# Kernel optimization log

Measured on AMD Instinct MI355X. Metric: run time of the kernel, lower is better.

The kernel has to match this reference:

```python
import jax, jax.numpy as jnp
import numpy as np

N = 10000      # nodes
E = 100000     # edges
C = 32         # in_channels == hidden_channels == out_channels
ED = 4         # edge_dim
G = 64         # number of graphs in the batch
EPS = 1e-5     # BatchNorm eps


def setup_inputs() -> dict:
    key = jax.random.key(0)
    ks = jax.random.split(key, 20)
    rn = lambda k, shape, s=0.05: jax.random.normal(k, shape, dtype=jnp.float32) * s
    return {
        "x": jax.random.normal(ks[0], (N, C), dtype=jnp.float32),
        "edge_attr": jax.random.normal(ks[1], (E, ED), dtype=jnp.float32),
        # edge MLP 1: ED -> C -> C*C ; NNConv1 root/bias
        "e1_w1": rn(ks[2], (ED, C)), "e1_b1": jnp.zeros((C,), jnp.float32),
        "e1_w2": rn(ks[3], (C, C * C)), "e1_b2": jnp.zeros((C * C,), jnp.float32),
        "root1": rn(ks[4], (C, C)), "bias1": jnp.zeros((C,), jnp.float32),
        # edge MLP 2: ED -> C -> C*C ; NNConv2 root/bias
        "e2_w1": rn(ks[5], (ED, C)), "e2_b1": jnp.zeros((C,), jnp.float32),
        "e2_w2": rn(ks[6], (C, C * C)), "e2_b2": jnp.zeros((C * C,), jnp.float32),
        "root2": rn(ks[7], (C, C)), "bias2": jnp.zeros((C,), jnp.float32),
        # BatchNorm (eval mode: running stats)
        "bn1_g": jnp.ones((C,), jnp.float32), "bn1_b": jnp.zeros((C,), jnp.float32),
        "bn1_m": rn(ks[8], (C,), 0.1), "bn1_v": 1.0 + 0.1 * jax.random.uniform(ks[9], (C,), dtype=jnp.float32),
        "bn2_g": jnp.ones((C,), jnp.float32), "bn2_b": jnp.zeros((C,), jnp.float32),
        "bn2_m": rn(ks[10], (C,), 0.1), "bn2_v": 1.0 + 0.1 * jax.random.uniform(ks[11], (C,), dtype=jnp.float32),
        # readout: C -> C//2 -> 1
        "r1_w": rn(ks[12], (C, C // 2)), "r1_b": jnp.zeros((C // 2,), jnp.float32),
        "r2_w": rn(ks[13], (C // 2, 1)), "r2_b": jnp.zeros((1,), jnp.float32),
        "edge_index": jax.random.randint(ks[14], (2, E), 0, N),
        "batch": jnp.sort(jax.random.randint(ks[15], (N,), 0, G)),
    }


def _nnconv(x, edge_index, edge_attr, w1, b1, w2, b2, root, bias):
    # edge MLP -> per-edge weight matrix [E, C, C]
    h = jax.nn.relu(edge_attr @ w1 + b1)
    W = (h @ w2 + b2).reshape(E, C, C)
    src, dst = edge_index[0], edge_index[1]
    # gather source features, per-edge matmul, scatter-mean to target nodes
    msg = jnp.einsum('ei,eio->eo', x[src], W)                      # [E, C]
    agg = jax.ops.segment_sum(msg, dst, num_segments=N)            # [N, C]
    cnt = jax.ops.segment_sum(jnp.ones((E,), x.dtype), dst, num_segments=N)
    agg = agg / jnp.maximum(cnt, 1.0)[:, None]
    return agg + x @ root + bias


def _bn(x, g, b, m, v):
    return (x - m) * jax.lax.rsqrt(v + EPS) * g + b


def reference(x, edge_attr,
              e1_w1, e1_b1, e1_w2, e1_b2, root1, bias1,
              e2_w1, e2_b1, e2_w2, e2_b2, root2, bias2,
              bn1_g, bn1_b, bn1_m, bn1_v,
              bn2_g, bn2_b, bn2_m, bn2_v,
              r1_w, r1_b, r2_w, r2_b,
              edge_index, batch):
    h = jax.nn.relu(_bn(_nnconv(x, edge_index, edge_attr, e1_w1, e1_b1, e1_w2, e1_b2, root1, bias1),
                        bn1_g, bn1_b, bn1_m, bn1_v))
    h = jax.nn.relu(_bn(_nnconv(h, edge_index, edge_attr, e2_w1, e2_b1, e2_w2, e2_b2, root2, bias2),
                        bn2_g, bn2_b, bn2_m, bn2_v))
    # global mean pool over graphs
    psum = jax.ops.segment_sum(h, batch, num_segments=G)           # [G, C]
    pcnt = jax.ops.segment_sum(jnp.ones((N,), h.dtype), batch, num_segments=G)
    pooled = psum / jnp.maximum(pcnt, 1.0)[:, None]
    # readout MLP (dropout is identity in eval)
    return jax.nn.relu(pooled @ r1_w + r1_b) @ r2_w + r2_b          # [G, 1]
```

## Files before the change

### kernel.cpp

```cpp
#include <hip/hip_runtime.h>

#define NN 10000
#define EE 100000
#define CC 32
#define GG 64
#define EPSV 1e-5f
#define NB 8
#define SLOTS 1056
#define HST 32
#define PST 36
#define PNODE (32*PST)
#define EBLK (EE/8)
#define HBLK ((EE+255)/256)
#define WBLK 160

__global__ __launch_bounds__(256) void k_pre(const int* __restrict__ ei,
        int* __restrict__ cnt, int* __restrict__ deg,
        const float* __restrict__ w2a, const float* __restrict__ b2a,
        const float* __restrict__ w2b, const float* __restrict__ b2b,
        float* __restrict__ w2r1, float* __restrict__ w2r2) {
    int blk = blockIdx.x;
    int t = threadIdx.x;
    if (blk < HBLK) {
        int e = blk * 256 + t;
        if (e < EE) {
            atomicAdd(&cnt[ei[EE + e]], 1);
            atomicAdd(&deg[ei[e]], 1);
        }
    } else {
        int b2i = blk - HBLK;
        int s = (b2i % 5) * 256 + t;
        int i = b2i / 5;
        if (s < SLOTS) {
            float va = (s < 1024) ? w2a[(s >> 5) * 1024 + i * 32 + (s & 31)]
                                  : b2a[i * 32 + (s - 1024)];
            float vb = (s < 1024) ? w2b[(s >> 5) * 1024 + i * 32 + (s & 31)]
                                  : b2b[i * 32 + (s - 1024)];
            w2r1[i * SLOTS + s] = va;
            w2r2[i * SLOTS + s] = vb;
        }
    }
}

__global__ __launch_bounds__(1024) void k_scan(const int* __restrict__ deg,
                                               int* __restrict__ rowptr,
                                               int* __restrict__ cursor) {
    __shared__ int buf[1024];
    int t = threadIdx.x;
    int v[10]; int s = 0;
    int base = t * 10;
    #pragma unroll
    for (int k = 0; k < 10; k++) {
        int idx = base + k;
        v[k] = (idx < NN) ? deg[idx] : 0;
        s += v[k];
    }
    buf[t] = s;
    for (int off = 1; off < 1024; off <<= 1) {
        __syncthreads();
        int val = buf[t] + ((t >= off) ? buf[t - off] : 0);
        __syncthreads();
        buf[t] = val;
    }
    __syncthreads();
    int carry = (t > 0) ? buf[t - 1] : 0;
    #pragma unroll
    for (int k = 0; k < 10; k++) {
        int idx = base + k;
        if (idx < NN) { rowptr[idx] = carry; cursor[idx] = carry; }
        carry += v[k];
    }
    if (t == 1023) rowptr[NN] = buf[1023];
}

__global__ void k_scatter(const int* __restrict__ ei,
                          int* __restrict__ cursor, int* __restrict__ csr_eid,
                          int2* __restrict__ meta) {
    int e = blockIdx.x * blockDim.x + threadIdx.x;
    if (e >= EE) return;
    int s = ei[e];
    int d = ei[EE + e];
    int pos = atomicAdd(&cursor[s], 1);
    csr_eid[pos] = e;
    meta[pos] = make_int2(s, d);
}

__global__ __launch_bounds__(256) void k_h(const float* __restrict__ edge_attr,
        const float* __restrict__ w1a, const float* __restrict__ b1a,
        const float* __restrict__ w1b, const float* __restrict__ b1b,
        const int* __restrict__ csr_eid,
        float* __restrict__ hbuf1, float* __restrict__ hbuf2) {
    int t = threadIdx.x;
    int pos = blockIdx.x * 8 + (t >> 5);
    int o = t & 31;
    int e = csr_eid[pos];
    float4 a = *(const float4*)&edge_attr[(size_t)e * 4];
    float ha = fmaxf(a.x * w1a[o] + a.y * w1a[32 + o] + a.z * w1a[64 + o] + a.w * w1a[96 + o] + b1a[o], 0.f);
    float hb = fmaxf(a.x * w1b[o] + a.y * w1b[32 + o] + a.z * w1b[64 + o] + a.w * w1b[96 + o] + b1b[o], 0.f);
    hbuf1[(size_t)pos * HST + o] = ha;
    hbuf2[(size_t)pos * HST + o] = hb;
}

__global__ __launch_bounds__(256, 3) void k_fused3(const float* __restrict__ x,
        const float* __restrict__ hbuf,
        const float* __restrict__ w2r,
        const int2* __restrict__ meta, const int* __restrict__ rowptr,
        float* __restrict__ agg) {
    __shared__ float xs[NB][32];
    __shared__ float P2[NB * PNODE];
    int t = threadIdx.x;
    int o = t & 31;
    int cb = 4 * (t >> 5);
    int n0 = blockIdx.x * NB;

    xs[t >> 5][t & 31] = x[n0 * 32 + t];
    __syncthreads();

    {
        float acc[4][NB];
        #pragma unroll
        for (int k = 0; k < 4; k++)
            #pragma unroll
            for (int n = 0; n < NB; n++) acc[k][n] = 0.f;
        #pragma unroll
        for (int j = 0; j < 8; j++) {
            float wk[4][4];
            #pragma unroll
            for (int r = 0; r < 4; r++)
                #pragma unroll
                for (int k = 0; k < 4; k++)
                    wk[r][k] = w2r[(4 * j + r) * SLOTS + (cb + k) * 32 + o];
            #pragma unroll
            for (int n = 0; n < NB; n++) {
                float4 xq = *(const float4*)&xs[n][4 * j];
                #pragma unroll
                for (int k = 0; k < 4; k++)
                    acc[k][n] += xq.x * wk[0][k] + xq.y * wk[1][k]
                               + xq.z * wk[2][k] + xq.w * wk[3][k];
            }
        }
        #pragma unroll
        for (int n = 0; n < NB; n++) {
            float4 st = make_float4(acc[0][n], acc[1][n], acc[2][n], acc[3][n]);
            *(float4*)&P2[n * PNODE + o * PST + cb] = st;
        }
    }
    if (t < 32) {
        float wb[32];
        #pragma unroll
        for (int i = 0; i < 32; i++) wb[i] = w2r[i * SLOTS + 1024 + t];
        #pragma unroll
        for (int n = 0; n < NB; n++) {
            float b = 0.f;
            #pragma unroll
            for (int j = 0; j < 8; j++) {
                float4 xq = *(const float4*)&xs[n][4 * j];
                b += xq.x * wb[4 * j] + xq.y * wb[4 * j + 1]
                   + xq.z * wb[4 * j + 2] + xq.w * wb[4 * j + 3];
            }
            *(float4*)&P2[n * PNODE + t * PST + 32] = make_float4(b, 0.f, 0.f, 0.f);
        }
    }
    __syncthreads();

    int ebase = rowptr[n0];
    int eend  = rowptr[n0 + NB];
    int grp = t >> 5;
    int pos = ebase + grp;
    int src_c = 0, dst_c = 0;
    float4 hq[8];
    if (pos < eend) {
        int2 sd = meta[pos];
        src_c = sd.x; dst_c = sd.y;
        const float* hb = &hbuf[(size_t)pos * HST];
        #pragma unroll
        for (int b = 0; b < 8; b++) hq[b] = *(const float4*)&hb[4 * b];
    }
    while (pos < eend) {
        int pos_n = pos + 8;
        int src_n = 0, dst_n = 0;
        float4 hq_n[8];
        if (pos_n < eend) {
            int2 sd = meta[pos_n];
            src_n = sd.x; dst_n = sd.y;
            const float* hbn = &hbuf[(size_t)pos_n * HST];
            #pragma unroll
            for (int b = 0; b < 8; b++) hq_n[b] = *(const float4*)&hbn[4 * b];
        }
        const float* Pn = &P2[(src_c - n0) * PNODE + o * PST];
        float msg = Pn[32];
        #pragma unroll
        for (int b = 0; b < 8; b++) {
            float4 pq = *(const float4*)&Pn[4 * b];
            msg += hq[b].x * pq.x + hq[b].y * pq.y
                 + hq[b].z * pq.z + hq[b].w * pq.w;
        }
        atomicAdd(&agg[(size_t)dst_c * 32 + o], msg);
        pos = pos_n; src_c = src_n; dst_c = dst_n;
        #pragma unroll
        for (int b = 0; b < 8; b++) hq[b] = hq_n[b];
    }
}

__global__ __launch_bounds__(256) void k_combine(const float* __restrict__ x_in,
        float* __restrict__ agg, const int* __restrict__ cnt,
        const float* __restrict__ root, const float* __restrict__ bias,
        const float* __restrict__ bng, const float* __restrict__ bnb,
        const float* __restrict__ bnm, const float* __restrict__ bnv,
        float* __restrict__ x_out, float* __restrict__ psum,
        const int* __restrict__ batch) {
    __shared__ float xs[8][32];
    __shared__ float vals[8][32];
    __shared__ int gb[8];
    int t = threadIdx.x;
    int n0 = blockIdx.x * 8;
    xs[t >> 5][t & 31] = x_in[n0 * 32 + t];
    __syncthreads();
    int k = t >> 5, o = t & 31, n = n0 + k;
    float r = bias[o];
    #pragma unroll
    for (int i = 0; i < 32; i++) r += xs[k][i] * root[i * 32 + o];
    float a = agg[(size_t)n * 32 + o] / fmaxf((float)cnt[n], 1.f);
    float val = a + r;
    val = (val - bnm[o]) * rsqrtf(bnv[o] + EPSV) * bng[o] + bnb[o];
    val = fmaxf(val, 0.f);
    if (x_out) {
        x_out[(size_t)n * 32 + o] = val;
        agg[(size_t)n * 32 + o] = 0.f;
    }
    if (psum) {
        vals[k][o] = val;
        if (o == 0) gb[k] = batch[n];
        __syncthreads();
        if (k == 0) {
            float acc = vals[0][o];
            int g = gb[0];
            #pragma unroll
            for (int k2 = 1; k2 < 8; k2++) {
                if (gb[k2] == g) acc += vals[k2][o];
                else {
                    atomicAdd(&psum[(size_t)g * 32 + o], acc);
                    g = gb[k2]; acc = vals[k2][o];
                }
            }
            atomicAdd(&psum[(size_t)g * 32 + o], acc);
        }
    }
}

__global__ __launch_bounds__(256) void k_readout(const float* __restrict__ psum,
        const int* __restrict__ batch,
        const float* __restrict__ r1w, const float* __restrict__ r1b,
        const float* __restrict__ r2w, const float* __restrict__ r2b,
        float* __restrict__ out) {
    __shared__ float w1s[32 * 16];
    __shared__ float b1s[16];
    __shared__ float w2s[16];
    __shared__ float ps[GG * 32];
    int t = threadIdx.x;
    int cnt_g = 0;
    if (t < GG) {
        int lo = 0, hi = NN;
        while (lo < hi) { int m = (lo + hi) >> 1; if (batch[m] < t) lo = m + 1; else hi = m; }
        int lb = lo;
        lo = 0; hi = NN;
        while (lo < hi) { int m = (lo + hi) >> 1; if (batch[m] < t + 1) lo = m + 1; else hi = m; }
        cnt_g = lo - lb;
    }
    w1s[t] = r1w[t];
    w1s[t + 256] = r1w[t + 256];
    if (t < 16) { b1s[t] = r1b[t]; w2s[t] = r2w[t]; }
    #pragma unroll
    for (int i = 0; i < GG * 32 / 256; i++) ps[t + i * 256] = psum[t + i * 256];
    __syncthreads();
    if (t < GG) {
        float inv = 1.f / fmaxf((float)cnt_g, 1.f);
        float acc = r2b[0];
        #pragma unroll
        for (int j = 0; j < 16; j++) {
            float dot = 0.f;
            #pragma unroll
            for (int c = 0; c < 32; c++) dot += ps[t * 32 + c] * w1s[c * 16 + j];
            float z = dot * inv + b1s[j];
            acc += fmaxf(z, 0.f) * w2s[j];
        }
        out[t] = acc;
    }
}

extern "C" void kernel_launch(void* const* d_in, const int* in_sizes, int n_in,
                              void* d_out, int out_size, void* d_ws, size_t ws_size,
                              hipStream_t stream) {
    const float* x       = (const float*)d_in[0];
    const float* eattr   = (const float*)d_in[1];
    const float* e1_w1   = (const float*)d_in[2];
    const float* e1_b1   = (const float*)d_in[3];
    const float* e1_w2   = (const float*)d_in[4];
    const float* e1_b2   = (const float*)d_in[5];
    const float* root1   = (const float*)d_in[6];
    const float* bias1   = (const float*)d_in[7];
    const float* e2_w1   = (const float*)d_in[8];
    const float* e2_b1   = (const float*)d_in[9];
    const float* e2_w2   = (const float*)d_in[10];
    const float* e2_b2   = (const float*)d_in[11];
    const float* root2   = (const float*)d_in[12];
    const float* bias2   = (const float*)d_in[13];
    const float* bn1_g   = (const float*)d_in[14];
    const float* bn1_b   = (const float*)d_in[15];
    const float* bn1_m   = (const float*)d_in[16];
    const float* bn1_v   = (const float*)d_in[17];
    const float* bn2_g   = (const float*)d_in[18];
    const float* bn2_b   = (const float*)d_in[19];
    const float* bn2_m   = (const float*)d_in[20];
    const float* bn2_v   = (const float*)d_in[21];
    const float* r1_w    = (const float*)d_in[22];
    const float* r1_b    = (const float*)d_in[23];
    const float* r2_w    = (const float*)d_in[24];
    const float* r2_b    = (const float*)d_in[25];
    const int*   ei      = (const int*)d_in[26];
    const int*   batch   = (const int*)d_in[27];

    char* ws = (char*)d_ws;
    float* hbuf1  = (float*)(ws);
    float* hbuf2  = (float*)(ws + 12800000);
    float* w2r1   = (float*)(ws + 25600000);
    float* w2r2   = (float*)(ws + 25735168);
    float* agg    = (float*)(ws + 25870336);
    int*   cnt    = (int*)  (ws + 27150336);
    int*   deg    = (int*)  (ws + 27190336);
    float* psum   = (float*)(ws + 27230336);
    float* xmid   = (float*)(ws + 27238528);
    int*   rowptr = (int*)  (ws + 28518528);
    int*   cursor = (int*)  (ws + 28558592);
    int*   csr    = (int*)  (ws + 28598592);
    int2*  meta   = (int2*) (ws + 28998592);

    hipMemsetAsync(ws + 25870336, 0, 1368192, stream);

    k_pre<<<HBLK + WBLK, 256, 0, stream>>>(ei, cnt, deg,
                                           e1_w2, e1_b2, e2_w2, e2_b2, w2r1, w2r2);
    k_scan<<<1, 1024, 0, stream>>>(deg, rowptr, cursor);
    k_scatter<<<(EE + 255) / 256, 256, 0, stream>>>(ei, cursor, csr, meta);
    k_h<<<EBLK, 256, 0, stream>>>(eattr, e1_w1, e1_b1, e2_w1, e2_b1, csr, hbuf1, hbuf2);

    k_fused3<<<NN / NB, 256, 0, stream>>>(x, hbuf1, w2r1, meta, rowptr, agg);
    k_combine<<<NN / 8, 256, 0, stream>>>(x, agg, cnt, root1, bias1,
                                          bn1_g, bn1_b, bn1_m, bn1_v,
                                          xmid, nullptr, batch);

    k_fused3<<<NN / NB, 256, 0, stream>>>(xmid, hbuf2, w2r2, meta, rowptr, agg);
    k_combine<<<NN / 8, 256, 0, stream>>>(xmid, agg, cnt, root2, bias2,
                                          bn2_g, bn2_b, bn2_m, bn2_v,
                                          nullptr, psum, batch);

    k_readout<<<1, 256, 0, stream>>>(psum, batch, r1_w, r1_b, r2_w, r2_b, (float*)d_out);
}
```

Measured before the change: 242.0 us.

## Fuse edge-MLP hidden computation into CSR scatter and prefetch edge data to LDS

Merges the edge hidden-layer computation into the CSR scatter kernel, so each edge thread computes both hidden vectors and writes them straight to its CSR slot. This removes the csr_eid indirection and one kernel launch. In the per-node-block message kernel, hidden rows and metadata for up to CAP edges are loaded into registers before the P2 precompute and staged into shared memory afterwards, hiding global latency behind that compute. The larger shared footprint lowers occupancy (launch bounds 3->2), and per-thread 32-wide hidden stores become uncoalesced strided float4 writes.

```diff
diff --git a/kernel.cpp b/kernel.cpp
--- a/kernel.cpp
+++ b/kernel.cpp
@@ -10,7 +10,7 @@
 #define HST 32
 #define PST 36
 #define PNODE (32*PST)
-#define EBLK (EE/8)
+#define CAP 144
 #define HBLK ((EE+255)/256)
 #define WBLK 160
 
@@ -73,45 +73,72 @@
     if (t == 1023) rowptr[NN] = buf[1023];
 }
 
-__global__ void k_scatter(const int* __restrict__ ei,
-                          int* __restrict__ cursor, int* __restrict__ csr_eid,
-                          int2* __restrict__ meta) {
-    int e = blockIdx.x * blockDim.x + threadIdx.x;
-    if (e >= EE) return;
-    int s = ei[e];
-    int d = ei[EE + e];
-    int pos = atomicAdd(&cursor[s], 1);
-    csr_eid[pos] = e;
-    meta[pos] = make_int2(s, d);
-}
-
-__global__ __launch_bounds__(256) void k_h(const float* __restrict__ edge_attr,
+__global__ __launch_bounds__(256) void k_scatter(const int* __restrict__ ei,
+        const float* __restrict__ edge_attr,
         const float* __restrict__ w1a, const float* __restrict__ b1a,
         const float* __restrict__ w1b, const float* __restrict__ b1b,
-        const int* __restrict__ csr_eid,
+        int* __restrict__ cursor, int2* __restrict__ meta,
         float* __restrict__ hbuf1, float* __restrict__ hbuf2) {
-    int t = threadIdx.x;
-    int pos = blockIdx.x * 8 + (t >> 5);
-    int o = t & 31;
-    int e = csr_eid[pos];
+    __shared__ float wsh[320];
+    int t = threadIdx.x;
+    for (int s = t; s < 320; s += 256) {
+        wsh[s] = (s < 128) ? w1a[s]
+               : (s < 160) ? b1a[s - 128]
+               : (s < 288) ? w1b[s - 160]
+                           : b1b[s - 288];
+    }
+    __syncthreads();
+    int e = blockIdx.x * 256 + t;
+    if (e >= EE) return;
+    int sn = ei[e];
+    int dn = ei[EE + e];
     float4 a = *(const float4*)&edge_attr[(size_t)e * 4];
-    float ha = fmaxf(a.x * w1a[o] + a.y * w1a[32 + o] + a.z * w1a[64 + o] + a.w * w1a[96 + o] + b1a[o], 0.f);
-    float hb = fmaxf(a.x * w1b[o] + a.y * w1b[32 + o] + a.z * w1b[64 + o] + a.w * w1b[96 + o] + b1b[o], 0.f);
-    hbuf1[(size_t)pos * HST + o] = ha;
-    hbuf2[(size_t)pos * HST + o] = hb;
-}
-
-__global__ __launch_bounds__(256, 3) void k_fused3(const float* __restrict__ x,
+    int pos = atomicAdd(&cursor[sn], 1);
+    meta[pos] = make_int2(sn, dn);
+    float h1v[32], h2v[32];
+    #pragma unroll
+    for (int o = 0; o < 32; o++) {
+        h1v[o] = fmaxf(a.x * wsh[o]       + a.y * wsh[32 + o]  + a.z * wsh[64 + o]  + a.w * wsh[96 + o]  + wsh[128 + o], 0.f);
+        h2v[o] = fmaxf(a.x * wsh[160 + o] + a.y * wsh[192 + o] + a.z * wsh[224 + o] + a.w * wsh[256 + o] + wsh[288 + o], 0.f);
+    }
+    #pragma unroll
+    for (int ob = 0; ob < 8; ob++) {
+        *(float4*)&hbuf1[(size_t)pos * HST + 4 * ob] =
+            make_float4(h1v[4 * ob], h1v[4 * ob + 1], h1v[4 * ob + 2], h1v[4 * ob + 3]);
+        *(float4*)&hbuf2[(size_t)pos * HST + 4 * ob] =
+            make_float4(h2v[4 * ob], h2v[4 * ob + 1], h2v[4 * ob + 2], h2v[4 * ob + 3]);
+    }
+}
+
+__global__ __launch_bounds__(256, 2) void k_fused3(const float* __restrict__ x,
         const float* __restrict__ hbuf,
         const float* __restrict__ w2r,
         const int2* __restrict__ meta, const int* __restrict__ rowptr,
         float* __restrict__ agg) {
     __shared__ float xs[NB][32];
     __shared__ float P2[NB * PNODE];
+    __shared__ float sh_h[CAP * HST];
+    __shared__ int2  sh_meta[CAP];
     int t = threadIdx.x;
     int o = t & 31;
     int cb = 4 * (t >> 5);
     int n0 = blockIdx.x * NB;
+
+    int ebase = rowptr[n0];
+    int eend  = rowptr[n0 + NB];
+    int ne    = eend - ebase;
+    int ne_st = (ne < CAP) ? ne : CAP;
+
+    const float4* hsrc = (const float4*)&hbuf[(size_t)ebase * HST];
+    int nvec = ne_st * (HST / 4);
+    float4 rv[5];
+    #pragma unroll
+    for (int k = 0; k < 5; k++) {
+        int vi = t + 256 * k;
+        if (vi < nvec) rv[k] = hsrc[vi];
+    }
+    int2 mv = make_int2(n0, 0);
+    if (t < ne_st) mv = meta[ebase + t];
 
     xs[t >> 5][t & 31] = x[n0 * 32 + t];
     __syncthreads();
@@ -161,44 +188,47 @@
             *(float4*)&P2[n * PNODE + t * PST + 32] = make_float4(b, 0.f, 0.f, 0.f);
         }
     }
-    __syncthreads();
-
-    int ebase = rowptr[n0];
-    int eend  = rowptr[n0 + NB];
+
+    {
+        float4* hdst = (float4*)sh_h;
+        #pragma unroll
+        for (int k = 0; k < 5; k++) {
+            int vi = t + 256 * k;
+            if (vi < nvec) hdst[vi] = rv[k];
+        }
+        if (t < ne_st) sh_meta[t] = mv;
+    }
+    __syncthreads();
+
     int grp = t >> 5;
-    int pos = ebase + grp;
-    int src_c = 0, dst_c = 0;
-    float4 hq[8];
-    if (pos < eend) {
-        int2 sd = meta[pos];
-        src_c = sd.x; dst_c = sd.y;
-        const float* hb = &hbuf[(size_t)pos * HST];
-        #pragma unroll
-        for (int b = 0; b < 8; b++) hq[b] = *(const float4*)&hb[4 * b];
-    }
-    while (pos < eend) {
-        int pos_n = pos + 8;
-        int src_n = 0, dst_n = 0;
-        float4 hq_n[8];
-        if (pos_n < eend) {
-            int2 sd = meta[pos_n];
-            src_n = sd.x; dst_n = sd.y;
-            const float* hbn = &hbuf[(size_t)pos_n * HST];
-            #pragma unroll
-            for (int b = 0; b < 8; b++) hq_n[b] = *(const float4*)&hbn[4 * b];
-        }
-        const float* Pn = &P2[(src_c - n0) * PNODE + o * PST];
+    int idx = grp;
+    int2 sd = make_int2(n0, 0);
+    if (idx < ne) sd = (idx < ne_st) ? sh_meta[idx] : meta[ebase + idx];
+    while (idx < ne) {
+        int idx_n = idx + 8;
+        int2 sd_n = sd;
+        if (idx_n < ne) sd_n = (idx_n < ne_st) ? sh_meta[idx_n] : meta[ebase + idx_n];
+        const float* Pn = &P2[(sd.x - n0) * PNODE + o * PST];
         float msg = Pn[32];
-        #pragma unroll
-        for (int b = 0; b < 8; b++) {
-            float4 pq = *(const float4*)&Pn[4 * b];
-            msg += hq[b].x * pq.x + hq[b].y * pq.y
-                 + hq[b].z * pq.z + hq[b].w * pq.w;
-        }
-        atomicAdd(&agg[(size_t)dst_c * 32 + o], msg);
-        pos = pos_n; src_c = src_n; dst_c = dst_n;
-        #pragma unroll
-        for (int b = 0; b < 8; b++) hq[b] = hq_n[b];
+        if (idx < ne_st) {
+            const float* hr = &sh_h[idx * HST];
+            #pragma unroll
+            for (int b = 0; b < 8; b++) {
+                float4 hqv = *(const float4*)&hr[4 * b];
+                float4 pq  = *(const float4*)&Pn[4 * b];
+                msg += hqv.x * pq.x + hqv.y * pq.y + hqv.z * pq.z + hqv.w * pq.w;
+            }
+        } else {
+            const float* hr = &hbuf[(size_t)(ebase + idx) * HST];
+            #pragma unroll
+            for (int b = 0; b < 8; b++) {
+                float4 hqv = *(const float4*)&hr[4 * b];
+                float4 pq  = *(const float4*)&Pn[4 * b];
+                msg += hqv.x * pq.x + hqv.y * pq.y + hqv.z * pq.z + hqv.w * pq.w;
+            }
+        }
+        atomicAdd(&agg[(size_t)sd.y * 32 + o], msg);
+        idx = idx_n; sd = sd_n;
     }
 }
 
@@ -332,16 +362,16 @@
     float* xmid   = (float*)(ws + 27238528);
     int*   rowptr = (int*)  (ws + 28518528);
     int*   cursor = (int*)  (ws + 28558592);
-    int*   csr    = (int*)  (ws + 28598592);
-    int2*  meta   = (int2*) (ws + 28998592);
+    int2*  meta   = (int2*) (ws + 28598592);
 
     hipMemsetAsync(ws + 25870336, 0, 1368192, stream);
 
     k_pre<<<HBLK + WBLK, 256, 0, stream>>>(ei, cnt, deg,
                                            e1_w2, e1_b2, e2_w2, e2_b2, w2r1, w2r2);
     k_scan<<<1, 1024, 0, stream>>>(deg, rowptr, cursor);
-    k_scatter<<<(EE + 255) / 256, 256, 0, stream>>>(ei, cursor, csr, meta);
-    k_h<<<EBLK, 256, 0, stream>>>(eattr, e1_w1, e1_b1, e2_w1, e2_b1, csr, hbuf1, hbuf2);
+    k_scatter<<<(EE + 255) / 256, 256, 0, stream>>>(ei, eattr,
+                                                    e1_w1, e1_b1, e2_w1, e2_b1,
+                                                    cursor, meta, hbuf1, hbuf2);
 
     k_fused3<<<NN / NB, 256, 0, stream>>>(x, hbuf1, w2r1, meta, rowptr, agg);
     k_combine<<<NN / 8, 256, 0, stream>>>(x, agg, cnt, root1, bias1,
```

Result: slower. 311.1 us (+28.5%).
